# Kernel tuning notes

Hardware: AMD Instinct MI355X
Metric: run time of the kernel (lower is better)

## Reference

```python
import jax, jax.numpy as jnp
import numpy as np

L, B, S, D, H, E = 3, 2, 2048, 1024, 16, 4
Dh = D // H  # 64
DF = E * D   # 4096


def _ln(x, g, b, eps=1e-5):
    m = jnp.mean(x, axis=-1, keepdims=True)
    v = jnp.mean(jnp.square(x - m), axis=-1, keepdims=True)
    return (x - m) * jax.lax.rsqrt(v + eps) * g + b


def setup_inputs() -> dict:
    key = jax.random.key(0)
    ks = jax.random.split(key, 12)
    s = 0.02
    f32 = jnp.float32
    return {
        "x":    jax.random.normal(ks[0], (B, S, D), f32),
        "Wq":   jax.random.normal(ks[1], (L, Dh, Dh), f32) * s,
        "Wk":   jax.random.normal(ks[2], (L, Dh, Dh), f32) * s,
        "Wv":   jax.random.normal(ks[3], (L, Dh, Dh), f32) * s,
        "Wo":   jax.random.normal(ks[4], (L, D, D), f32) * s,
        "bo":   jnp.zeros((L, D), f32),
        "ln1_g": jnp.ones((L, D), f32),
        "ln1_b": jnp.zeros((L, D), f32),
        "W1":   jax.random.normal(ks[5], (L, DF, D), f32) * s,
        "b1":   jnp.zeros((L, DF), f32),
        "W2":   jax.random.normal(ks[6], (L, D, DF), f32) * s,
        "b2":   jnp.zeros((L, D), f32),
        "ln2_g": jnp.ones((L, D), f32),
        "ln2_b": jnp.zeros((L, D), f32),
    }


def reference(x, Wq, Wk, Wv, Wo, bo, ln1_g, ln1_b, W1, b1, W2, b2, ln2_g, ln2_b):
    scale = 1.0 / np.sqrt(Dh).astype(np.float32)
    out = x
    for l in range(L):
        xh = out.reshape(B, S, H, Dh)
        # per-head Linear (shared 64x64 weight across heads), torch Linear: y = x @ W.T
        q = jnp.einsum('bshd,ed->bhse', xh, Wq[l])  # [B,H,S,Dh]
        k = jnp.einsum('bshd,ed->bhse', xh, Wk[l])
        v = jnp.einsum('bshd,ed->bhse', xh, Wv[l])
        att = jax.nn.softmax(jnp.einsum('bhse,bhte->bhst', q, k) * scale, axis=-1)
        ctx = jnp.einsum('bhst,bhtd->bshd', att, v).reshape(B, S, D)
        att_out = ctx @ Wo[l].T + bo[l]
        n1 = _ln(att_out + out, ln1_g[l], ln1_b[l])  # residual adds layer input (v == out)
        ff = jax.nn.relu(n1 @ W1[l].T + b1[l]) @ W2[l].T + b2[l]
        out = _ln(ff + n1, ln2_g[l], ln2_b[l])
    return out
```

## Files before the change

### kernel.cpp

```cpp
#include <hip/hip_runtime.h>
#include <hip/hip_bf16.h>
#include <math.h>


#define DEVINL __device__ __forceinline__
typedef unsigned short ushort_t;
using short8 = __attribute__((ext_vector_type(8))) short;
using f32x4  = __attribute__((ext_vector_type(4))) float;

#if defined(__has_builtin)
#if __has_builtin(__builtin_amdgcn_exp2f)
#define EXPFN(x) __builtin_amdgcn_exp2f(x)
#define QSCALE 0.18033688011112042f
#define HAVE_EXP2 1
#endif
#endif
#ifndef HAVE_EXP2
#define EXPFN(x) __expf(x)
#define QSCALE 0.125f
#endif

DEVINL short f2b(float f) {
  unsigned u = __float_as_uint(f);
  u += 0x7fff + ((u >> 16) & 1);
  return (short)(u >> 16);
}
DEVINL unsigned pk2(float a, float b) {
  unsigned ua = __float_as_uint(a), ub = __float_as_uint(b);
  ua += 0x7fff + ((ua >> 16) & 1);
  ub += 0x7fff + ((ub >> 16) & 1);
  return (ua >> 16) | (ub & 0xffff0000u);
}
DEVINL unsigned pkc(float a, float b) {
  float2 f; f.x = a; f.y = b;
  __hip_bfloat162 h = __float22bfloat162_rn(f);
  return *reinterpret_cast<unsigned*>(&h);
}
DEVINL float bl(unsigned u) { return __uint_as_float(u << 16); }
DEVINL float bh(unsigned u) { return __uint_as_float(u & 0xffff0000u); }
DEVINL f32x4 mfma16(short8 a, short8 b, f32x4 c) {
  return __builtin_amdgcn_mfma_f32_16x16x32_bf16(a, b, c, 0, 0, 0);
}

typedef __attribute__((address_space(3))) void lds_void;
typedef __attribute__((address_space(1))) void gbl_void;
DEVINL void gl16(const void* g, void* l) {
  __builtin_amdgcn_global_load_lds((const gbl_void*)(unsigned long long)g,
                                   (lds_void*)(unsigned long long)l, 16, 0, 0);
}
template <int N> DEVINL void waitvm() {
  asm volatile("s_waitcnt vmcnt(%0)" ::"n"(N) : "memory");
}
DEVINL void barrier_raw() { __builtin_amdgcn_s_barrier(); }
DEVINL void sched0() { __builtin_amdgcn_sched_barrier(0); }
DEVINL void waitlgkm0() {
  asm volatile("s_waitcnt lgkmcnt(0)" ::: "memory");
}

__global__ __launch_bounds__(256)
void conv_bf16(const float* __restrict__ src, ushort_t* __restrict__ dst,
               int n8) {
  int i = blockIdx.x * 256 + threadIdx.x;
  const int stride = gridDim.x * 256;
  for (; i < n8; i += stride) {
    float4 a = ((const float4*)src)[2 * i];
    float4 b = ((const float4*)src)[2 * i + 1];
    uint4 o;
    o.x = pk2(a.x, a.y); o.y = pk2(a.z, a.w);
    o.z = pk2(b.x, b.y); o.w = pk2(b.z, b.w);
    ((uint4*)dst)[i] = o;
  }
}

DEVINL float block_sum(float v, float* red) {
#pragma unroll
  for (int off = 32; off > 0; off >>= 1) v += __shfl_xor(v, off, 64);
  if ((threadIdx.x & 63) == 0) red[threadIdx.x >> 6] = v;
  __syncthreads();
  float r = red[0] + red[1] + red[2] + red[3];
  __syncthreads();
  return r;
}

template <bool WF>
__global__ __launch_bounds__(256)
void ln_fuse(const ushort_t* __restrict__ pa, const ushort_t* __restrict__ pb,
             const float* __restrict__ bias, const ushort_t* __restrict__ Rb,
             const float* __restrict__ g, const float* __restrict__ b,
             ushort_t* __restrict__ outb, float* __restrict__ outf) {
  __shared__ float red[4];
  const size_t base = (size_t)blockIdx.x * 1024 + threadIdx.x * 4;
  uint2 ua = *(const uint2*)(pa + base);
  uint2 ub = *(const uint2*)(pb + base);
  uint2 ur = *(const uint2*)(Rb + base);
  float4 vbi = *(const float4*)(bias + threadIdx.x * 4);
  float4 v;
  v.x = bl(ua.x) + bl(ub.x) + bl(ur.x) + vbi.x;
  v.y = bh(ua.x) + bh(ub.x) + bh(ur.x) + vbi.y;
  v.z = bl(ua.y) + bl(ub.y) + bl(ur.y) + vbi.z;
  v.w = bh(ua.y) + bh(ub.y) + bh(ur.y) + vbi.w;
  float s = block_sum(v.x + v.y + v.z + v.w, red);
  float mean = s * (1.0f / 1024.0f);
  float dx = v.x - mean, dy = v.y - mean, dz = v.z - mean, dw = v.w - mean;
  float sq = block_sum(dx * dx + dy * dy + dz * dz + dw * dw, red);
  float rstd = rsqrtf(sq * (1.0f / 1024.0f) + 1e-5f);
  const float4 gv = *(const float4*)(g + threadIdx.x * 4);
  const float4 bv = *(const float4*)(b + threadIdx.x * 4);
  float4 o;
  o.x = dx * rstd * gv.x + bv.x;
  o.y = dy * rstd * gv.y + bv.y;
  o.z = dz * rstd * gv.z + bv.z;
  o.w = dw * rstd * gv.w + bv.w;
  uint2 p;
  p.x = pk2(o.x, o.y); p.y = pk2(o.z, o.w);
  *(uint2*)(outb + base) = p;
  if (WF) *(float4*)(outf + base) = o;
}

template <int BM, int BN, int WR, int WC, bool OBF, int EPI, bool SWZ>
__global__ __launch_bounds__(WR * WC * 64)
void gemm_db(const ushort_t* __restrict__ A, const ushort_t* __restrict__ W,
             const float* __restrict__ bias, void* __restrict__ Cp, int M,
             int N, int Klen, int lda, int ldw) {
  constexpr int THREADS = WR * WC * 64;
  constexpr int FM = BM / WR / 16;
  constexpr int FN = BN / WC / 16;
  constexpr int CA = BM * 8 / THREADS;
  constexpr int CB = BN * 8 / THREADS;
  constexpr int L = CA + CB;
  __shared__ __align__(16) ushort_t As[2][BM * 64];
  __shared__ __align__(16) ushort_t Bs[2][BN * 64];
  const int tid = threadIdx.x;
  const int lane = tid & 63, lo = lane & 15, hi = lane >> 4, w = tid >> 6;
  int bx = blockIdx.x, by = blockIdx.y;
  if (SWZ) {
    int id = by * gridDim.x + bx;
    const int cpx = (gridDim.x * gridDim.y) >> 3;
    id = (id & 7) * cpx + (id >> 3);
    bx = id % gridDim.x;
    by = id / gridDim.x;
  }
  const int m0 = by * BM, n0 = bx * BN;
  const int wm = (w / WC) * (BM / WR), wn = (w % WC) * (BN / WC);
  const int kbase = blockIdx.z * Klen;

  auto stage = [&](int t, int buf) {
    const int k0 = kbase + t * 64;
#pragma unroll
    for (int i = 0; i < CA; ++i) {
      const int c = i * THREADS + tid;
      const int r = c >> 3, sg = (c & 7) ^ (r & 7);
      gl16(A + (size_t)(m0 + r) * lda + k0 + sg * 8, &As[buf][c * 8]);
    }
#pragma unroll
    for (int i = 0; i < CB; ++i) {
      const int c = i * THREADS + tid;
      const int r = c >> 3, sg = (c & 7) ^ (r & 7);
      gl16(W + (size_t)(n0 + r) * ldw + k0 + sg * 8, &Bs[buf][c * 8]);
    }
  };

  f32x4 acc[FM][FN] = {};
  auto compute = [&](int cur) {
#pragma unroll
    for (int ks = 0; ks < 2; ++ks) {
      short8 af[FM], bf_[FN];
#pragma unroll
      for (int fm = 0; fm < FM; ++fm) {
        const int row = wm + fm * 16 + lo;
        af[fm] = *(const short8*)
            &As[cur][row * 64 + (((ks * 4 + hi) ^ (row & 7)) << 3)];
      }
#pragma unroll
      for (int fn = 0; fn < FN; ++fn) {
        const int row = wn + fn * 16 + lo;
        bf_[fn] = *(const short8*)
            &Bs[cur][row * 64 + (((ks * 4 + hi) ^ (row & 7)) << 3)];
      }
#pragma unroll
      for (int fm = 0; fm < FM; ++fm)
#pragma unroll
        for (int fn = 0; fn < FN; ++fn)
          acc[fm][fn] = mfma16(af[fm], bf_[fn], acc[fm][fn]);
    }
  };

  const int nt = Klen / 64;
  stage(0, 0);
  for (int t = 0; t < nt - 1; ++t) {
    const int cur = t & 1;
    stage(t + 1, cur ^ 1);
    waitvm<L>();
    barrier_raw(); sched0();
    compute(cur);
    barrier_raw(); sched0();
  }
  waitvm<0>();
  barrier_raw(); sched0();
  compute((nt - 1) & 1);

  float bv[FN];
#pragma unroll
  for (int fn = 0; fn < FN; ++fn)
    bv[fn] = (EPI & 1) ? bias[n0 + wn + fn * 16 + lo] : 0.f;
#pragma unroll
  for (int fm = 0; fm < FM; ++fm)
#pragma unroll
    for (int fn = 0; fn < FN; ++fn) {
      const int col = n0 + wn + fn * 16 + lo;
#pragma unroll
      for (int r = 0; r < 4; ++r) {
        const int row = m0 + wm + fm * 16 + hi * 4 + r;
        float v = acc[fm][fn][r] + bv[fn];
        if (EPI & 4) v = fmaxf(v, 0.f);
        if (OBF) {
          ushort_t* Cb = (ushort_t*)Cp + (size_t)blockIdx.z * M * N;
          Cb[(size_t)row * N + col] = (ushort_t)f2b(v);
        } else {
          float* Cf = (float*)Cp + (size_t)blockIdx.z * M * N;
          Cf[(size_t)row * N + col] = v;
        }
      }
    }
}

template <int EPI, bool SWZ>
__global__ __launch_bounds__(512, 2)
void gemm_8p(const ushort_t* __restrict__ A, const ushort_t* __restrict__ W,
             const float* __restrict__ bias, ushort_t* __restrict__ Cp, int M,
             int N, int K, int lda, int ldw) {
  __shared__ __align__(16) ushort_t As[2][256 * 64];
  __shared__ __align__(16) ushort_t Bs[2][256 * 64];
  const int tid = threadIdx.x;
  const int lane = tid & 63, lo = lane & 15, hi = lane >> 4, w = tid >> 6;
  const int wr = w >> 2, wc = w & 3;
  int bx = blockIdx.x, by = blockIdx.y;
  if (SWZ) {
    int id = by * gridDim.x + bx;
    const int cpx = (gridDim.x * gridDim.y) >> 3;
    id = (id & 7) * cpx + (id >> 3);
    bx = id % gridDim.x;
    by = id / gridDim.x;
  }
  const int m0 = by * 256, n0 = bx * 256;
  const int wm = wr * 128, wn = wc * 64;

  const int c0 = tid, c1 = 512 + tid;
  const int r0 = c0 >> 3, g0 = ((c0 & 7) ^ (r0 & 7)) << 3;
  const int r1 = c1 >> 3, g1 = ((c1 & 7) ^ (r1 & 7)) << 3;

  auto stA = [&](int tile, int half, int buf) {
    const ushort_t* s = A + (size_t)(m0 + half * 128) * lda + tile * 64;
    ushort_t* d = &As[buf][half * 128 * 64];
    gl16(s + (size_t)r0 * lda + g0, d + c0 * 8);
    gl16(s + (size_t)r1 * lda + g1, d + c1 * 8);
  };
  auto stB = [&](int tile, int half, int buf) {
    const ushort_t* s = W + (size_t)(n0 + half * 128) * ldw + tile * 64;
    ushort_t* d = &Bs[buf][half * 128 * 64];
    gl16(s + (size_t)r0 * ldw + g0, d + c0 * 8);
    gl16(s + (size_t)r1 * ldw + g1, d + c1 * 8);
  };

  f32x4 acc[8][4] = {};
  short8 af[2][4], bfA[2][2], bfB[2][2];

  auto ldA = [&](int buf, int qr) {
#pragma unroll
    for (int ks = 0; ks < 2; ++ks)
#pragma unroll
      for (int fm = 0; fm < 4; ++fm) {
        const int row = wm + qr * 64 + fm * 16 + lo;
        af[ks][fm] = *(const short8*)
            &As[buf][row * 64 + (((ks * 4 + hi) ^ (row & 7)) << 3)];
      }
  };
  auto ldB = [&](int buf, int qc, short8 (&bf)[2][2]) {
#pragma unroll
    for (int ks = 0; ks < 2; ++ks)
#pragma unroll
      for (int fn = 0; fn < 2; ++fn) {
        const int row = wn + qc * 32 + fn * 16 + lo;
        bf[ks][fn] = *(const short8*)
            &Bs[buf][row * 64 + (((ks * 4 + hi) ^ (row & 7)) << 3)];
      }
  };
  auto mmaQ = [&](auto qr, auto qc, short8 (&bf)[2][2]) {
    constexpr int QR = decltype(qr)::value, QC = decltype(qc)::value;
    __builtin_amdgcn_s_setprio(1);
#pragma unroll
    for (int ks = 0; ks < 2; ++ks)
#pragma unroll
      for (int fm = 0; fm < 4; ++fm)
#pragma unroll
        for (int fn = 0; fn < 2; ++fn)
          acc[QR * 4 + fm][QC * 2 + fn] = mfma16(
              af[ks][fm], bf[ks][fn], acc[QR * 4 + fm][QC * 2 + fn]);
    __builtin_amdgcn_s_setprio(0);
  };
  using I0 = std::integral_constant<int, 0>;
  using I1 = std::integral_constant<int, 1>;

  const int nt = K / 64;
  const int ni = nt / 2;

  stA(0, 0, 0); stA(0, 1, 0); stB(0, 0, 0); stB(0, 1, 0);
  stB(1, 0, 1); stB(1, 1, 1);
  waitvm<4>();
  barrier_raw();

  for (int j = 0; j < ni; ++j) {
    const int t1 = 2 * j + 1, t2 = 2 * j + 2, t3 = 2 * j + 3;
    const bool s2 = t2 < nt, s3 = t3 < nt;
    const bool last = (j == ni - 1);
    ldA(0, 0); ldB(0, 0, bfA);
    stA(t1, 0, 1);
    barrier_raw(); waitlgkm0(); sched0();
    mmaQ(I0{}, I0{}, bfA);
    barrier_raw();
    ldB(0, 1, bfB);
    stA(t1, 1, 1);
    barrier_raw(); waitlgkm0(); sched0();
    mmaQ(I0{}, I1{}, bfB);
    barrier_raw();
    ldA(0, 1);
    if (s2) stB(t2, 0, 0);
    barrier_raw(); waitlgkm0(); sched0();
    mmaQ(I1{}, I1{}, bfB);
    barrier_raw();
    if (s2) stB(t2, 1, 0);
    if (last) waitvm<0>(); else waitvm<4>();
    barrier_raw();
    mmaQ(I1{}, I0{}, bfA);
    barrier_raw();
    ldA(1, 0); ldB(1, 0, bfA);
    if (s2) stA(t2, 0, 0);
    barrier_raw(); waitlgkm0(); sched0();
    mmaQ(I0{}, I0{}, bfA);
    barrier_raw();
    ldB(1, 1, bfB);
    if (s2) stA(t2, 1, 0);
    barrier_raw(); waitlgkm0(); sched0();
    mmaQ(I0{}, I1{}, bfB);
    barrier_raw();
    ldA(1, 1);
    if (s3) stB(t3, 0, 1);
    barrier_raw(); waitlgkm0(); sched0();
    mmaQ(I1{}, I1{}, bfB);
    barrier_raw();
    if (s3) stB(t3, 1, 1);
    if (last) waitvm<0>(); else waitvm<4>();
    barrier_raw();
    mmaQ(I1{}, I0{}, bfA);
    barrier_raw();
  }

  float bv[4];
#pragma unroll
  for (int fn = 0; fn < 4; ++fn)
    bv[fn] = (EPI & 1) ? bias[n0 + wn + fn * 16 + lo] : 0.f;
#pragma unroll
  for (int fm = 0; fm < 8; ++fm)
#pragma unroll
    for (int fn = 0; fn < 4; ++fn) {
      const int col = n0 + wn + fn * 16 + lo;
#pragma unroll
      for (int r = 0; r < 4; ++r) {
        const int row = m0 + wm + fm * 16 + hi * 4 + r;
        float v = acc[fm][fn][r] + bv[fn];
        if (EPI & 4) v = fmaxf(v, 0.f);
        Cp[(size_t)row * N + col] = (ushort_t)f2b(v);
      }
    }
}

__global__ __launch_bounds__(256)
void qkv_kernel(const ushort_t* __restrict__ A, const ushort_t* __restrict__ Wq,
                const ushort_t* __restrict__ Wk, const ushort_t* __restrict__ Wv,
                ushort_t* __restrict__ q, ushort_t* __restrict__ k,
                ushort_t* __restrict__ v) {
  __shared__ __align__(16) ushort_t As[128 * 64];
  __shared__ __align__(16) ushort_t Ws[3][64 * 64];
  const int tid = threadIdx.x;
  const int lane = tid & 63, lo = lane & 15, hi = lane >> 4, w = tid >> 6;
  const int m0 = blockIdx.x * 128;
  const int wm = (w >> 1) * 64, wn = (w & 1) * 32;

#pragma unroll
  for (int i = 0; i < 4; ++i) {
    const int c = i * 256 + tid;
    const int r = c >> 3, sg = (c & 7) ^ (r & 7);
    gl16(A + (size_t)(m0 + r) * 64 + sg * 8, As + c * 8);
  }
#pragma unroll
  for (int o = 0; o < 3; ++o) {
    const ushort_t* wb = (o == 0) ? Wq : (o == 1) ? Wk : Wv;
#pragma unroll
    for (int i = 0; i < 2; ++i) {
      const int c = i * 256 + tid;
      const int r = c >> 3, sg = (c & 7) ^ (r & 7);
      gl16(wb + (size_t)r * 64 + sg * 8, Ws[o] + c * 8);
    }
  }
  __syncthreads();

#pragma unroll
  for (int o = 0; o < 3; ++o) {
    ushort_t* ob = (o == 0) ? q : (o == 1) ? k : v;
    const float sc = (o == 0) ? QSCALE : 1.0f;
    f32x4 acc[4][2] = {};
#pragma unroll
    for (int ks = 0; ks < 2; ++ks) {
      short8 af[4], bf[2];
#pragma unroll
      for (int fm = 0; fm < 4; ++fm) {
        const int row = wm + fm * 16 + lo;
        af[fm] = *(const short8*)
            &As[row * 64 + (((ks * 4 + hi) ^ (row & 7)) << 3)];
      }
#pragma unroll
      for (int fn = 0; fn < 2; ++fn) {
        const int row = wn + fn * 16 + lo;
        bf[fn] = *(const short8*)
            &Ws[o][row * 64 + (((ks * 4 + hi) ^ (row & 7)) << 3)];
      }
#pragma unroll
      for (int fm = 0; fm < 4; ++fm)
#pragma unroll
        for (int fn = 0; fn < 2; ++fn)
          acc[fm][fn] = mfma16(af[fm], bf[fn], acc[fm][fn]);
    }
#pragma unroll
    for (int fm = 0; fm < 4; ++fm)
#pragma unroll
      for (int fn = 0; fn < 2; ++fn) {
        const int col = wn + fn * 16 + lo;
#pragma unroll
        for (int r = 0; r < 4; ++r) {
          const int row = m0 + wm + fm * 16 + hi * 4 + r;
          size_t idx;
          if (o == 2) {
            idx = (size_t)row * 64 + col;
          } else {
            idx = (size_t)((row >> 15) * 16 + (row & 15)) * 131072 +
                  (size_t)((row >> 4) & 2047) * 64 + col;
          }
          ob[idx] = (ushort_t)f2b(acc[fm][fn][r] * sc);
        }
      }
  }
}

__global__ __launch_bounds__(256)
void vtrans(const ushort_t* __restrict__ V, ushort_t* __restrict__ VT) {
  __shared__ ushort_t T[64][65];
  const int tid = threadIdx.x;
  const int s0 = blockIdx.x * 64, hd0 = blockIdx.y * 64, b = blockIdx.z;
  const ushort_t* src = V + (size_t)b * 2097152;
  ushort_t* dst = VT + (size_t)b * 2097152;
#pragma unroll
  for (int i = 0; i < 2; ++i) {
    int c = tid + i * 256;
    int s = c >> 3, kg = c & 7;
    short8 hv = *(const short8*)(src + (size_t)(s0 + s) * 1024 + hd0 + kg * 8);
#pragma unroll
    for (int j = 0; j < 8; ++j) T[s][kg * 8 + j] = (ushort_t)hv[j];
  }
  __syncthreads();
#pragma unroll
  for (int i = 0; i < 2; ++i) {
    int c = tid + i * 256;
    int hd = c >> 3, sg = c & 7;
    short8 o;
#pragma unroll
    for (int j = 0; j < 8; ++j) o[j] = (short)T[sg * 8 + j][hd];
    *(short8*)(dst + (size_t)(hd0 + hd) * 2048 + s0 + sg * 8) = o;
  }
}

__global__ __launch_bounds__(256)
void attn4(const ushort_t* __restrict__ Qh, const ushort_t* __restrict__ Kh,
           const ushort_t* __restrict__ VT, ushort_t* __restrict__ O) {
  __shared__ __align__(16) ushort_t Kbuf[2][64 * 64];
  __shared__ __align__(16) ushort_t Vbuf[2][64 * 64];
  __shared__ __align__(16) ushort_t Pbuf[4][2][16 * 40];
  const int tid = threadIdx.x, w = tid >> 6, lane = tid & 63;
  const int lo = lane & 15, hi = lane >> 4;
  const int hid = blockIdx.y * 16 + blockIdx.x;
  const int logical = (hid & 7) * 64 + (hid >> 3);
  const int bh = logical >> 4, qt = logical & 15;
  const int b = bh >> 4, h = bh & 15;
  const size_t hq = (size_t)bh * 131072;
  const size_t vth = (size_t)b * 2097152 + (size_t)h * 131072;
  const size_t oh = (size_t)b * 2097152 + (size_t)h * 64;
  const int qrow = qt * 128 + w * 32;
  ushort_t* Pa = Pbuf[w][0];
  ushort_t* Pb = Pbuf[w][1];

  const ushort_t* qpa = Qh + hq + (size_t)(qrow + lo) * 64 + hi * 8;
  const short8 qf0a = *(const short8*)qpa;
  const short8 qf1a = *(const short8*)(qpa + 32);
  const short8 qf0b = *(const short8*)(qpa + 1024);
  const short8 qf1b = *(const short8*)(qpa + 1024 + 32);

  const int c0 = tid, c1 = 256 + tid;
  const int r0 = c0 >> 3, s0 = ((c0 & 7) ^ (r0 & 7)) << 3;
  const int r1 = c1 >> 3, s1 = ((c1 & 7) ^ (r1 & 7)) << 3;
  const ushort_t* kg0 = Kh + hq + (size_t)r0 * 64 + s0;
  const ushort_t* kg1 = Kh + hq + (size_t)r1 * 64 + s1;
  const ushort_t* vg0 = VT + vth + (size_t)r0 * 2048 + s0;
  const ushort_t* vg1 = VT + vth + (size_t)r1 * 2048 + s1;

  auto stage = [&](int kt, int buf) {
    gl16(kg0 + (size_t)kt * 4096, &Kbuf[buf][c0 * 8]);
    gl16(kg1 + (size_t)kt * 4096, &Kbuf[buf][c1 * 8]);
    gl16(vg0 + kt * 64, &Vbuf[buf][c0 * 8]);
    gl16(vg1 + kt * 64, &Vbuf[buf][c1 * 8]);
  };

  f32x4 acca[4] = {}, accb[4] = {};
  f32x4 la = {}, lb = {};
  const int sw = lo & 7;
  const int ko0 = (hi ^ sw) << 3, ko1 = ((4 + hi) ^ sw) << 3;

  auto body = [&](const ushort_t* Kc, const ushort_t* Vc) {
    f32x4 sa[4], sb[4];
#pragma unroll
    for (int fm = 0; fm < 4; ++fm) {
      const int rb = (fm * 16 + lo) * 64;
      short8 k0 = *(const short8*)&Kc[rb + ko0];
      short8 k1 = *(const short8*)&Kc[rb + ko1];
      f32x4 ta = {};
      ta = mfma16(k0, qf0a, ta);
      ta = mfma16(k1, qf1a, ta);
      sa[fm] = ta;
      f32x4 tb = {};
      tb = mfma16(k0, qf0b, tb);
      tb = mfma16(k1, qf1b, tb);
      sb[fm] = tb;
    }
    short8 vf[4][2];
#pragma unroll
    for (int fn = 0; fn < 4; ++fn) {
      const int rb = (fn * 16 + lo) * 64;
      vf[fn][0] = *(const short8*)&Vc[rb + ko0];
      vf[fn][1] = *(const short8*)&Vc[rb + ko1];
    }
#pragma unroll
    for (int fm = 0; fm < 4; ++fm) {
      f32x4 p;
      p[0] = EXPFN(sa[fm][0]); p[1] = EXPFN(sa[fm][1]);
      p[2] = EXPFN(sa[fm][2]); p[3] = EXPFN(sa[fm][3]);
      la += p;
      uint2 pw;
      pw.x = pkc(p[0], p[1]); pw.y = pkc(p[2], p[3]);
      *(uint2*)&Pa[lo * 40 + fm * 16 + hi * 4] = pw;
      f32x4 r;
      r[0] = EXPFN(sb[fm][0]); r[1] = EXPFN(sb[fm][1]);
      r[2] = EXPFN(sb[fm][2]); r[3] = EXPFN(sb[fm][3]);
      lb += r;
      uint2 rw;
      rw.x = pkc(r[0], r[1]); rw.y = pkc(r[2], r[3]);
      *(uint2*)&Pb[lo * 40 + fm * 16 + hi * 4] = rw;
    }
    short8 pa0 = *(const short8*)&Pa[lo * 40 + hi * 8];
    short8 pa1 = *(const short8*)&Pa[lo * 40 + 32 + hi * 8];
    short8 pb0 = *(const short8*)&Pb[lo * 40 + hi * 8];
    short8 pb1 = *(const short8*)&Pb[lo * 40 + 32 + hi * 8];
#pragma unroll
    for (int fn = 0; fn < 4; ++fn) {
      acca[fn] = mfma16(vf[fn][0], pa0, acca[fn]);
      acca[fn] = mfma16(vf[fn][1], pa1, acca[fn]);
      accb[fn] = mfma16(vf[fn][0], pb0, accb[fn]);
      accb[fn] = mfma16(vf[fn][1], pb1, accb[fn]);
    }
  };

  stage(0, 0);
  __syncthreads();
  for (int kt2 = 0; kt2 < 16; ++kt2) {
    stage(2 * kt2 + 1, 1);
    body(Kbuf[0], Vbuf[0]);
    __syncthreads();
    if (kt2 < 15) stage(2 * kt2 + 2, 0);
    body(Kbuf[1], Vbuf[1]);
    __syncthreads();
  }

  float lsa = (la[0] + la[1]) + (la[2] + la[3]);
  lsa += __shfl_xor(lsa, 16);
  lsa += __shfl_xor(lsa, 32);
  float lsb = (lb[0] + lb[1]) + (lb[2] + lb[3]);
  lsb += __shfl_xor(lsb, 16);
  lsb += __shfl_xor(lsb, 32);
  const float inva = 1.0f / lsa, invb = 1.0f / lsb;
  ushort_t* opa = O + oh + (size_t)(qrow + lo) * 1024 + hi * 4;
  ushort_t* opb = opa + 16 * 1024;
#pragma unroll
  for (int fn = 0; fn < 4; ++fn) {
    uint2 oa, ob;
    oa.x = pk2(acca[fn][0] * inva, acca[fn][1] * inva);
    oa.y = pk2(acca[fn][2] * inva, acca[fn][3] * inva);
    ob.x = pk2(accb[fn][0] * invb, accb[fn][1] * invb);
    ob.y = pk2(accb[fn][2] * invb, accb[fn][3] * invb);
    *(uint2*)(opa + fn * 16) = oa;
    *(uint2*)(opb + fn * 16) = ob;
  }
}

extern "C" void kernel_launch(void* const* d_in, const int* in_sizes, int n_in,
                              void* d_out, int out_size, void* d_ws,
                              size_t ws_size, hipStream_t stream) {
  const float* x    = (const float*)d_in[0];
  const float* Wq   = (const float*)d_in[1];
  const float* Wk   = (const float*)d_in[2];
  const float* Wv   = (const float*)d_in[3];
  const float* Wo   = (const float*)d_in[4];
  const float* bo   = (const float*)d_in[5];
  const float* ln1g = (const float*)d_in[6];
  const float* ln1b = (const float*)d_in[7];
  const float* W1   = (const float*)d_in[8];
  const float* b1   = (const float*)d_in[9];
  const float* W2   = (const float*)d_in[10];
  const float* b2   = (const float*)d_in[11];
  const float* ln2g = (const float*)d_in[12];
  const float* ln2b = (const float*)d_in[13];
  float* out = (float*)d_out;
  char* wsb = (char*)d_ws;

  ushort_t* t0  = (ushort_t*)wsb;
  ushort_t* t0b = t0 + 4194304;
  ushort_t* q   = (ushort_t*)(wsb + (16ull << 20));
  ushort_t* k   = (ushort_t*)(wsb + (24ull << 20));
  ushort_t* v   = (ushort_t*)(wsb + (32ull << 20));
  ushort_t* vt  = (ushort_t*)(wsb + (40ull << 20));
  ushort_t* ff  = q;
  ushort_t* ctx = (ushort_t*)(wsb + (48ull << 20));
  ushort_t* n1b = ctx;
  ushort_t* xbf = (ushort_t*)(wsb + (56ull << 20));
  ushort_t* wqb = (ushort_t*)(wsb + (64ull << 20));
  ushort_t* wkb = wqb + 3 * 4096;
  ushort_t* wvb = wkb + 3 * 4096;
  ushort_t* wob = (ushort_t*)(wsb + (65ull << 20));
  ushort_t* w1b = (ushort_t*)(wsb + (72ull << 20));
  ushort_t* w2b = (ushort_t*)(wsb + (96ull << 20));

  auto conv = [&](const float* s, ushort_t* d, long n) {
    int n8 = (int)(n / 8);
    int g = (n8 + 255) / 256;
    if (g > 2048) g = 2048;
    conv_bf16<<<g, 256, 0, stream>>>(s, d, n8);
  };
  conv(x, xbf, 4194304);
  conv(Wq, wqb, 3 * 4096);
  conv(Wk, wkb, 3 * 4096);
  conv(Wv, wvb, 3 * 4096);
  conv(Wo, wob, 3ll * 1048576);
  conv(W1, w1b, 3ll * 4194304);
  conv(W2, w2b, 3ll * 4194304);

  const ushort_t* curb = xbf;
  for (int l = 0; l < 3; ++l) {
    qkv_kernel<<<512, 256, 0, stream>>>(curb, wqb + l * 4096, wkb + l * 4096,
                                        wvb + l * 4096, q, k, v);
    vtrans<<<dim3(32, 16, 2), 256, 0, stream>>>(v, vt);
    attn4<<<dim3(16, 32), 256, 0, stream>>>(q, k, vt, ctx);
    gemm_db<128, 128, 2, 2, true, 0, true>
        <<<dim3(8, 32, 2), 256, 0, stream>>>(ctx, wob + (size_t)l * 1048576,
                                             nullptr, t0, 4096, 1024, 512,
                                             1024, 1024);
    ln_fuse<false><<<4096, 256, 0, stream>>>(t0, t0b, bo + l * 1024, curb,
                                             ln1g + l * 1024, ln1b + l * 1024,
                                             n1b, nullptr);
    gemm_8p<5, true><<<dim3(16, 16), 512, 0, stream>>>(
        n1b, w1b + (size_t)l * 4194304, b1 + l * 4096, ff, 4096, 4096, 1024,
        1024, 1024);
    gemm_db<128, 128, 2, 2, true, 0, true>
        <<<dim3(8, 32, 2), 256, 0, stream>>>(ff, w2b + (size_t)l * 4194304,
                                             nullptr, t0, 4096, 1024, 2048,
                                             4096, 4096);
    if (l == 2)
      ln_fuse<true><<<4096, 256, 0, stream>>>(t0, t0b, b2 + l * 1024, n1b,
                                              ln2g + l * 1024, ln2b + l * 1024,
                                              xbf, out);
    else
      ln_fuse<false><<<4096, 256, 0, stream>>>(t0, t0b, b2 + l * 1024, n1b,
                                               ln2g + l * 1024, ln2b + l * 1024,
                                               xbf, nullptr);
    curb = xbf;
  }
}
```

Measured before the change: 525.4 us.

## Split attention across KV halves with a combine kernel

Attention now launches twice as many blocks, each covering half of the key sequence. Each block writes unnormalized bf16 partial outputs and row sums, and a new combine kernel adds the two halves and normalizes them. The body also reuses one P buffer per wave, which halves that LDS allocation and may raise occupancy. The cost is an extra launch, an extra read and write of the output, and bf16 rounding of the unnormalized partials. Since the softmax has no max subtraction, summing the two halves directly is exact.

```diff
diff --git a/kernel.cpp b/kernel.cpp
--- a/kernel.cpp
+++ b/kernel.cpp
@@ -479,13 +479,19 @@
 }
 
 __global__ __launch_bounds__(256)
-void attn4(const ushort_t* __restrict__ Qh, const ushort_t* __restrict__ Kh,
-           const ushort_t* __restrict__ VT, ushort_t* __restrict__ O) {
+void attn5(const ushort_t* __restrict__ Qh, const ushort_t* __restrict__ Kh,
+           const ushort_t* __restrict__ VT, ushort_t* __restrict__ O0,
+           ushort_t* __restrict__ O1, float* __restrict__ L0,
+           float* __restrict__ L1) {
   __shared__ __align__(16) ushort_t Kbuf[2][64 * 64];
   __shared__ __align__(16) ushort_t Vbuf[2][64 * 64];
-  __shared__ __align__(16) ushort_t Pbuf[4][2][16 * 40];
+  __shared__ __align__(16) ushort_t Pbuf[4][16 * 40];
   const int tid = threadIdx.x, w = tid >> 6, lane = tid & 63;
   const int lo = lane & 15, hi = lane >> 4;
+  const int z = blockIdx.z;
+  ushort_t* O = z ? O1 : O0;
+  float* L = z ? L1 : L0;
+  const int ktb = z * 16;
   const int hid = blockIdx.y * 16 + blockIdx.x;
   const int logical = (hid & 7) * 64 + (hid >> 3);
   const int bh = logical >> 4, qt = logical & 15;
@@ -494,8 +500,7 @@
   const size_t vth = (size_t)b * 2097152 + (size_t)h * 131072;
   const size_t oh = (size_t)b * 2097152 + (size_t)h * 64;
   const int qrow = qt * 128 + w * 32;
-  ushort_t* Pa = Pbuf[w][0];
-  ushort_t* Pb = Pbuf[w][1];
+  ushort_t* Pw = Pbuf[w];
 
   const ushort_t* qpa = Qh + hq + (size_t)(qrow + lo) * 64 + hi * 8;
   const short8 qf0a = *(const short8*)qpa;
@@ -512,10 +517,11 @@
   const ushort_t* vg1 = VT + vth + (size_t)r1 * 2048 + s1;
 
   auto stage = [&](int kt, int buf) {
-    gl16(kg0 + (size_t)kt * 4096, &Kbuf[buf][c0 * 8]);
-    gl16(kg1 + (size_t)kt * 4096, &Kbuf[buf][c1 * 8]);
-    gl16(vg0 + kt * 64, &Vbuf[buf][c0 * 8]);
-    gl16(vg1 + kt * 64, &Vbuf[buf][c1 * 8]);
+    const int kg = ktb + kt;
+    gl16(kg0 + (size_t)kg * 4096, &Kbuf[buf][c0 * 8]);
+    gl16(kg1 + (size_t)kg * 4096, &Kbuf[buf][c1 * 8]);
+    gl16(vg0 + kg * 64, &Vbuf[buf][c0 * 8]);
+    gl16(vg1 + kg * 64, &Vbuf[buf][c1 * 8]);
   };
 
   f32x4 acca[4] = {}, accb[4] = {};
@@ -554,23 +560,29 @@
       la += p;
       uint2 pw;
       pw.x = pkc(p[0], p[1]); pw.y = pkc(p[2], p[3]);
-      *(uint2*)&Pa[lo * 40 + fm * 16 + hi * 4] = pw;
+      *(uint2*)&Pw[lo * 40 + fm * 16 + hi * 4] = pw;
+    }
+    short8 pa0 = *(const short8*)&Pw[lo * 40 + hi * 8];
+    short8 pa1 = *(const short8*)&Pw[lo * 40 + 32 + hi * 8];
+#pragma unroll
+    for (int fn = 0; fn < 4; ++fn) {
+      acca[fn] = mfma16(vf[fn][0], pa0, acca[fn]);
+      acca[fn] = mfma16(vf[fn][1], pa1, acca[fn]);
+    }
+#pragma unroll
+    for (int fm = 0; fm < 4; ++fm) {
       f32x4 r;
       r[0] = EXPFN(sb[fm][0]); r[1] = EXPFN(sb[fm][1]);
       r[2] = EXPFN(sb[fm][2]); r[3] = EXPFN(sb[fm][3]);
       lb += r;
       uint2 rw;
       rw.x = pkc(r[0], r[1]); rw.y = pkc(r[2], r[3]);
-      *(uint2*)&Pb[lo * 40 + fm * 16 + hi * 4] = rw;
-    }
-    short8 pa0 = *(const short8*)&Pa[lo * 40 + hi * 8];
-    short8 pa1 = *(const short8*)&Pa[lo * 40 + 32 + hi * 8];
-    short8 pb0 = *(const short8*)&Pb[lo * 40 + hi * 8];
-    short8 pb1 = *(const short8*)&Pb[lo * 40 + 32 + hi * 8];
+      *(uint2*)&Pw[lo * 40 + fm * 16 + hi * 4] = rw;
+    }
+    short8 pb0 = *(const short8*)&Pw[lo * 40 + hi * 8];
+    short8 pb1 = *(const short8*)&Pw[lo * 40 + 32 + hi * 8];
 #pragma unroll
     for (int fn = 0; fn < 4; ++fn) {
-      acca[fn] = mfma16(vf[fn][0], pa0, acca[fn]);
-      acca[fn] = mfma16(vf[fn][1], pa1, acca[fn]);
       accb[fn] = mfma16(vf[fn][0], pb0, accb[fn]);
       accb[fn] = mfma16(vf[fn][1], pb1, accb[fn]);
     }
@@ -578,11 +590,11 @@
 
   stage(0, 0);
   __syncthreads();
-  for (int kt2 = 0; kt2 < 16; ++kt2) {
+  for (int kt2 = 0; kt2 < 8; ++kt2) {
     stage(2 * kt2 + 1, 1);
     body(Kbuf[0], Vbuf[0]);
     __syncthreads();
-    if (kt2 < 15) stage(2 * kt2 + 2, 0);
+    if (kt2 < 7) stage(2 * kt2 + 2, 0);
     body(Kbuf[1], Vbuf[1]);
     __syncthreads();
   }
@@ -593,19 +605,42 @@
   float lsb = (lb[0] + lb[1]) + (lb[2] + lb[3]);
   lsb += __shfl_xor(lsb, 16);
   lsb += __shfl_xor(lsb, 32);
-  const float inva = 1.0f / lsa, invb = 1.0f / lsb;
+  if (hi == 0) {
+    L[bh * 2048 + qrow + lo] = lsa;
+    L[bh * 2048 + qrow + 16 + lo] = lsb;
+  }
   ushort_t* opa = O + oh + (size_t)(qrow + lo) * 1024 + hi * 4;
   ushort_t* opb = opa + 16 * 1024;
 #pragma unroll
   for (int fn = 0; fn < 4; ++fn) {
     uint2 oa, ob;
-    oa.x = pk2(acca[fn][0] * inva, acca[fn][1] * inva);
-    oa.y = pk2(acca[fn][2] * inva, acca[fn][3] * inva);
-    ob.x = pk2(accb[fn][0] * invb, accb[fn][1] * invb);
-    ob.y = pk2(accb[fn][2] * invb, accb[fn][3] * invb);
+    oa.x = pk2(acca[fn][0], acca[fn][1]);
+    oa.y = pk2(acca[fn][2], acca[fn][3]);
+    ob.x = pk2(accb[fn][0], accb[fn][1]);
+    ob.y = pk2(accb[fn][2], accb[fn][3]);
     *(uint2*)(opa + fn * 16) = oa;
     *(uint2*)(opb + fn * 16) = ob;
   }
+}
+
+__global__ __launch_bounds__(256)
+void attn_combine(const ushort_t* __restrict__ O0,
+                  const ushort_t* __restrict__ O1,
+                  const float* __restrict__ L0, const float* __restrict__ L1,
+                  ushort_t* __restrict__ C) {
+  const int bs = blockIdx.x;
+  const int tid = threadIdx.x;
+  const int b = bs >> 11, s = bs & 2047;
+  const int h = tid >> 4;
+  const size_t base = (size_t)bs * 1024 + tid * 4;
+  const int lrow = (b * 16 + h) * 2048 + s;
+  const float inv = 1.0f / (L0[lrow] + L1[lrow]);
+  uint2 ua = *(const uint2*)(O0 + base);
+  uint2 ub = *(const uint2*)(O1 + base);
+  uint2 o;
+  o.x = pk2((bl(ua.x) + bl(ub.x)) * inv, (bh(ua.x) + bh(ub.x)) * inv);
+  o.y = pk2((bl(ua.y) + bl(ub.y)) * inv, (bh(ua.y) + bh(ub.y)) * inv);
+  *(uint2*)(C + base) = o;
 }
 
 extern "C" void kernel_launch(void* const* d_in, const int* in_sizes, int n_in,
@@ -642,6 +677,8 @@
   ushort_t* wkb = wqb + 3 * 4096;
   ushort_t* wvb = wkb + 3 * 4096;
   ushort_t* wob = (ushort_t*)(wsb + (65ull << 20));
+  float*    ls0 = (float*)(wsb + (71ull << 20));
+  float*    ls1 = ls0 + 65536;
   ushort_t* w1b = (ushort_t*)(wsb + (72ull << 20));
   ushort_t* w2b = (ushort_t*)(wsb + (96ull << 20));
 
@@ -664,7 +701,8 @@
     qkv_kernel<<<512, 256, 0, stream>>>(curb, wqb + l * 4096, wkb + l * 4096,
                                         wvb + l * 4096, q, k, v);
     vtrans<<<dim3(32, 16, 2), 256, 0, stream>>>(v, vt);
-    attn4<<<dim3(16, 32), 256, 0, stream>>>(q, k, vt, ctx);
+    attn5<<<dim3(16, 32, 2), 256, 0, stream>>>(q, k, vt, ctx, t0, ls0, ls1);
+    attn_combine<<<4096, 256, 0, stream>>>(ctx, t0, ls0, ls1, ctx);
     gemm_db<128, 128, 2, 2, true, 0, true>
         <<<dim3(8, 32, 2), 256, 0, stream>>>(ctx, wob + (size_t)l * 1048576,
                                              nullptr, t0, 4096, 1024, 512,
```

Result: slower. 544.5 us (+3.6%).
